# Performance work log

Hardware: AMD Instinct MI355X
Metric: run time of the kernel (lower is better)

## Reference

```python
import jax, jax.numpy as jnp
import numpy as np

N_NODES = 50000
N_EDGES = 800000
IN_C, HID_C, OUT_C = 128, 128, 64


def setup_inputs() -> dict:
    key = jax.random.key(0)
    k1, k2, k3, k4, k5 = jax.random.split(key, 5)
    x = jax.random.normal(k1, (N_NODES, IN_C), dtype=jnp.float32)
    edge_index = jax.random.randint(k2, (2, N_EDGES), 0, N_NODES, dtype=jnp.int64)
    # Glorot-style init for GCN weights, zero bias (PyG GCNConv defaults)
    s1 = (6.0 / (IN_C + HID_C)) ** 0.5
    s2 = (6.0 / (HID_C + OUT_C)) ** 0.5
    W1 = jax.random.uniform(k3, (IN_C, HID_C), jnp.float32, -s1, s1)
    W2 = jax.random.uniform(k4, (HID_C, OUT_C), jnp.float32, -s2, s2)
    b1 = jnp.zeros((HID_C,), jnp.float32)
    b2 = jnp.zeros((OUT_C,), jnp.float32)
    return {"x": x, "edge_index": edge_index, "W1": W1, "b1": b1, "W2": W2, "b2": b2}


def _gcn_conv(x, src, dst, W, b, n_nodes):
    # PyG GCNConv: add self-loops, symmetric normalization, linear transform,
    # scatter-add aggregation from src (row) to dst (col), then bias.
    h = x @ W  # [N, out]
    loops = jnp.arange(n_nodes, dtype=src.dtype)
    src_f = jnp.concatenate([src, loops])
    dst_f = jnp.concatenate([dst, loops])
    deg = jax.ops.segment_sum(jnp.ones_like(dst_f, dtype=h.dtype), dst_f,
                              num_segments=n_nodes)  # in-degree incl. self-loop
    dinv = jnp.where(deg > 0, jax.lax.rsqrt(deg), 0.0)
    norm = dinv[src_f] * dinv[dst_f]  # [E + N]
    msgs = h[src_f] * norm[:, None]   # gather + scale
    out = jax.ops.segment_sum(msgs, dst_f, num_segments=n_nodes)  # scatter-add
    return out + b


def reference(x, edge_index, W1, b1, W2, b2):
    src, dst = edge_index[0], edge_index[1]
    n = x.shape[0]
    h = jax.nn.relu(_gcn_conv(x, src, dst, W1, b1, n))
    return _gcn_conv(h, src, dst, W2, b2, n)
```

## Files before the change

### kernel.cpp

```cpp
#include <hip/hip_runtime.h>
#include <hip/hip_bf16.h>
#include <hip/hip_fp16.h>


#define NBUCK 800
#define CHUNK 2048
#define STASH 2048

typedef float f32x4 __attribute__((ext_vector_type(4)));
typedef _Float16 f16x8 __attribute__((ext_vector_type(8)));

__global__ __launch_bounds__(256) void presort_k(const int* __restrict__ src,
                                                 const int* __restrict__ dst,
                                                 unsigned* __restrict__ rec2,
                                                 int* __restrict__ hist2,
                                                 int* __restrict__ runstart2,
                                                 int E) {
    __shared__ int lh[NBUCK], lscan[NBUCK], cur[NBUCK];
    __shared__ int sred[256];
    __shared__ unsigned srec[CHUNK];
    int t = threadIdx.x;
    int lo = blockIdx.x * CHUNK, hi = min(E, lo + CHUNK);

    for (int i = t; i < NBUCK; i += 256) lh[i] = 0;
    __syncthreads();
    for (int e = lo + t; e < hi; e += 256)
        atomicAdd(&lh[dst[e] >> 6], 1);
    __syncthreads();

    int base = t * 4;
    int v[4];
    int s = 0;
#pragma unroll
    for (int i = 0; i < 4; ++i) {
        int idx = base + i;
        int c = (idx < NBUCK) ? lh[idx] : 0;
        v[i] = c; s += c;
    }
    sred[t] = s;
    __syncthreads();
#pragma unroll
    for (int off = 1; off < 256; off <<= 1) {
        int x = 0;
        if (t >= off) x = sred[t - off];
        __syncthreads();
        sred[t] += x;
        __syncthreads();
    }
    int run = sred[t] - s;
#pragma unroll
    for (int i = 0; i < 4; ++i) {
        int idx = base + i;
        if (idx < NBUCK) { lscan[idx] = run; cur[idx] = run; }
        run += v[i];
    }
    __syncthreads();

    for (int e = lo + t; e < hi; e += 256) {
        int d = dst[e];
        int p = atomicAdd(&cur[d >> 6], 1);
        srec[p] = (unsigned)(src[e] & 0xffff) | ((unsigned)d << 16);
    }
    __syncthreads();

    int n = hi - lo;
    for (int j = t; j < n; j += 256) rec2[lo + j] = srec[j];
    int hbase = blockIdx.x * NBUCK;
    for (int b = t; b < NBUCK; b += 256) {
        hist2[hbase + b] = lh[b];
        runstart2[hbase + b] = lscan[b];
    }
}

__global__ __launch_bounds__(256) void coltot_k(const int* __restrict__ hist2,
                                                int* __restrict__ btot, int BCNT) {
    __shared__ int sred[256];
    int b = blockIdx.x, t = threadIdx.x;
    int s = 0;
    for (int i = t; i < BCNT; i += 256) s += hist2[i * NBUCK + b];
    sred[t] = s;
    __syncthreads();
#pragma unroll
    for (int off = 128; off > 0; off >>= 1) {
        if (t < off) sred[t] += sred[t + off];
        __syncthreads();
    }
    if (t == 0) btot[b] = sred[0];
}

__global__ __launch_bounds__(256) void finish2_k(const unsigned* __restrict__ rec2,
                                                 const int* __restrict__ hist2,
                                                 const int* __restrict__ runstart2,
                                                 const int* __restrict__ btot,
                                                 int* __restrict__ offsets,
                                                 float* __restrict__ dinv,
                                                 unsigned short* __restrict__ adj,
                                                 int BCNT, int N, int E) {
    __shared__ int ncnt[64], ncur[64], nodeOff[64];
    __shared__ int stashCnt;
    __shared__ int sred[256];
    __shared__ unsigned stash[STASH];
    __shared__ unsigned short adjl[STASH];
    int b = blockIdx.x, t = threadIdx.x;
    if (t < 64) { ncnt[t] = 0; ncur[t] = 0; }
    if (t == 0) stashCnt = 0;
    if (b == 0 && t == 0) offsets[N] = E;

    int ps = 0;
    for (int i = t; i < b; i += 256) ps += btot[i];
    sred[t] = ps;
    __syncthreads();
#pragma unroll
    for (int off = 128; off > 0; off >>= 1) {
        if (t < off) sred[t] += sred[t + off];
        __syncthreads();
    }
    int bstart = sred[0];
    __syncthreads();

    for (int i = t; i < BCNT; i += 256) {
        int len = hist2[i * NBUCK + b];
        if (!len) continue;
        int gbase = i * CHUNK + runstart2[i * NBUCK + b];
        int sp = atomicAdd(&stashCnt, len);
        for (int k = 0; k < len; ++k) {
            unsigned r = rec2[gbase + k];
            atomicAdd(&ncnt[(r >> 16) & 63], 1);
            if (sp + k < STASH) stash[sp + k] = r;
        }
    }
    __syncthreads();

    if (t == 0) {
        int r = 0;
#pragma unroll
        for (int i = 0; i < 64; ++i) { nodeOff[i] = r; r += ncnt[i]; }
    }
    __syncthreads();

    if (t < 64) {
        int gnode = b * 64 + t;
        if (gnode < N) {
            dinv[gnode] = rsqrtf((float)(ncnt[t] + 1));
            offsets[gnode] = bstart + nodeOff[t];
        }
    }
    __syncthreads();

    int tot = stashCnt;
    if (tot > STASH) tot = STASH;
    for (int j = t; j < tot; j += 256) {
        unsigned r = stash[j];
        int ln = (r >> 16) & 63;
        int p = atomicAdd(&ncur[ln], 1);
        adjl[nodeOff[ln] + p] = (unsigned short)(r & 0xffff);
    }
    __syncthreads();
    for (int j = t; j < tot; j += 256) adj[bstart + j] = adjl[j];
}

template <int NOUT, bool HALF_IN>
__global__ __launch_bounds__(256) void gemm_mfma_k(const void* __restrict__ Xv,
                                                   const float* __restrict__ W,
                                                   const float* __restrict__ dinv,
                                                   __half* __restrict__ Hout, int M) {
    constexpr int K = 128;
    constexpr int BM = 64;
    constexpr int LDP = K + 8;
    constexpr int CT = NOUT / 16;
    __shared__ _Float16 xs[BM][LDP];
    __shared__ _Float16 wsl[NOUT][LDP];

    int t = threadIdx.x;
    int brow = blockIdx.x * BM;

    if constexpr (HALF_IN) {
        const __half* X = (const __half*)Xv;
        for (int i = t; i < BM * (K / 8); i += 256) {
            int row = i / (K / 8), c8 = i % (K / 8);
            int gr = brow + row;
            union { _Float16 h[8]; uint4 u; } pk;
            if (gr < M) {
                uint4 u = *(const uint4*)(X + (size_t)gr * K + c8 * 8);
                const __half2* hp = (const __half2*)&u;
                float di = dinv[gr];
#pragma unroll
                for (int j = 0; j < 4; ++j) {
                    float2 f = __half22float2(hp[j]);
                    pk.h[2 * j] = (_Float16)(f.x * di);
                    pk.h[2 * j + 1] = (_Float16)(f.y * di);
                }
            } else {
                pk.u = make_uint4(0, 0, 0, 0);
            }
            *(uint4*)&xs[row][c8 * 8] = pk.u;
        }
    } else {
        const float* X = (const float*)Xv;
        for (int i = t; i < BM * (K / 4); i += 256) {
            int row = i / (K / 4), c4 = i % (K / 4);
            int gr = brow + row;
            union { _Float16 h[4]; uint2 u; } pk;
            if (gr < M) {
                float4 v = *(const float4*)(X + (size_t)gr * K + c4 * 4);
                float di = dinv[gr];
                pk.h[0] = (_Float16)(v.x * di);
                pk.h[1] = (_Float16)(v.y * di);
                pk.h[2] = (_Float16)(v.z * di);
                pk.h[3] = (_Float16)(v.w * di);
            } else {
                pk.u = make_uint2(0, 0);
            }
            *(uint2*)&xs[row][c4 * 4] = pk.u;
        }
    }

    for (int i = t; i < K * (NOUT / 4); i += 256) {
        int k = i / (NOUT / 4), c4 = i % (NOUT / 4);
        float4 wv = *(const float4*)(W + (size_t)k * NOUT + c4 * 4);
        wsl[c4 * 4 + 0][k] = (_Float16)wv.x;
        wsl[c4 * 4 + 1][k] = (_Float16)wv.y;
        wsl[c4 * 4 + 2][k] = (_Float16)wv.z;
        wsl[c4 * 4 + 3][k] = (_Float16)wv.w;
    }
    __syncthreads();

    int w = t >> 6, lane = t & 63;
    int lrow = lane & 15;
    int lko = (lane >> 4) * 8;

    f32x4 acc[CT];
#pragma unroll
    for (int c = 0; c < CT; ++c) acc[c] = (f32x4){0.f, 0.f, 0.f, 0.f};

#pragma unroll
    for (int s = 0; s < K / 32; ++s) {
        f16x8 a = *(const f16x8*)&xs[w * 16 + lrow][s * 32 + lko];
#pragma unroll
        for (int c = 0; c < CT; ++c) {
            f16x8 b = *(const f16x8*)&wsl[c * 16 + lrow][s * 32 + lko];
            acc[c] = __builtin_amdgcn_mfma_f32_16x16x32_f16(a, b, acc[c], 0, 0, 0);
        }
    }

    __syncthreads();
#pragma unroll
    for (int c = 0; c < CT; ++c) {
#pragma unroll
        for (int r = 0; r < 4; ++r)
            xs[w * 16 + (lane >> 4) * 4 + r][c * 16 + lrow] = (_Float16)acc[c][r];
    }
    __syncthreads();
    for (int j = t; j < BM * (NOUT / 8); j += 256) {
        int row = j / (NOUT / 8), c8 = j % (NOUT / 8);
        int gr = brow + row;
        if (gr < M)
            *(uint4*)(Hout + (size_t)gr * NOUT + c8 * 8) = *(uint4*)&xs[row][c8 * 8];
    }
}

__device__ __forceinline__ void ld_row(const __half* p, float (&f)[4]) {
    uint2 u = *(const uint2*)p;
    const __half2* hp = (const __half2*)&u;
    float2 a = __half22float2(hp[0]);
    float2 b = __half22float2(hp[1]);
    f[0] = a.x; f[1] = a.y; f[2] = b.x; f[3] = b.y;
}
__device__ __forceinline__ void ld_row(const __half* p, float (&f)[2]) {
    float2 a = __half22float2(*(const __half2*)p);
    f[0] = a.x; f[1] = a.y;
}

template <int C, bool RELU, typename TOUT>
__global__ __launch_bounds__(256) void aggregate_k(const __half* __restrict__ H,
                                                   const int* __restrict__ offsets,
                                                   const unsigned short* __restrict__ adj,
                                                   const float* __restrict__ dinv,
                                                   const float* __restrict__ bias,
                                                   TOUT* __restrict__ out, int n) {
    constexpr int V = C / 32;
    int wave = threadIdx.x >> 6;
    int lane = threadIdx.x & 63;
    int half_id = lane >> 5;
    int sub = lane & 31;
    int node = blockIdx.x * 8 + wave * 2 + half_id;
    if (node >= n) return;

    const __half* hl = H + sub * V;

    float acc[V];
    ld_row(hl + (size_t)node * C, acc);

    int e0 = offsets[node], e1 = offsets[node + 1];
    int e = e0;

    for (; e + 8 <= e1; e += 8) {
        int s[8];
#pragma unroll
        for (int j = 0; j < 8; ++j) s[j] = adj[e + j];
        float t[8][V];
#pragma unroll
        for (int j = 0; j < 8; ++j) ld_row(hl + (size_t)s[j] * C, t[j]);
#pragma unroll
        for (int v = 0; v < V; ++v)
            acc[v] += ((t[0][v] + t[1][v]) + (t[2][v] + t[3][v])) +
                      ((t[4][v] + t[5][v]) + (t[6][v] + t[7][v]));
    }
    for (; e + 2 <= e1; e += 2) {
        int s0 = adj[e], s1 = adj[e + 1];
        float t0[V], t1[V];
        ld_row(hl + (size_t)s0 * C, t0);
        ld_row(hl + (size_t)s1 * C, t1);
#pragma unroll
        for (int v = 0; v < V; ++v) acc[v] += t0[v] + t1[v];
    }
    if (e < e1) {
        float t0[V];
        ld_row(hl + (size_t)adj[e] * C, t0);
#pragma unroll
        for (int v = 0; v < V; ++v) acc[v] += t0[v];
    }

    float di = dinv[node];
    float o[V];
#pragma unroll
    for (int v = 0; v < V; ++v) {
        o[v] = acc[v] * di + bias[sub * V + v];
        if (RELU) o[v] = fmaxf(o[v], 0.f);
    }

    if constexpr (sizeof(TOUT) == 2) {
        union { __half2 h[2]; uint2 u; } pk;
        pk.h[0] = __floats2half2_rn(o[0], o[1]);
        pk.h[1] = __floats2half2_rn(o[2], o[3]);
        *(uint2*)((__half*)out + (size_t)node * C + sub * V) = pk.u;
    } else {
        *(float2*)((float*)out + (size_t)node * C + sub * V) = make_float2(o[0], o[1]);
    }
}

extern "C" void kernel_launch(void* const* d_in, const int* in_sizes, int n_in,
                              void* d_out, int out_size, void* d_ws, size_t ws_size,
                              hipStream_t stream) {
    const float* x = (const float*)d_in[0];
    const int* ei = (const int*)d_in[1];
    const float* W1 = (const float*)d_in[2];
    const float* b1 = (const float*)d_in[3];
    const float* W2 = (const float*)d_in[4];
    const float* b2 = (const float*)d_in[5];
    float* out = (float*)d_out;

    const int IN_C = 128, HID_C = 128;
    int N = in_sizes[0] / IN_C;
    int E = in_sizes[1] / 2;
    const int* src = ei;
    const int* dst = ei + E;

    int BCNT = (E + CHUNK - 1) / CHUNK;

    int NP = (N + 255) & ~255;
    int EP = (E + 255) & ~255;
    char* w = (char*)d_ws;
    int* hist2 = (int*)w;           w += (size_t)BCNT * NBUCK * 4;
    int* runstart2 = (int*)w;       w += (size_t)BCNT * NBUCK * 4;
    int* btot = (int*)w;            w += (size_t)(NBUCK + 32) * 4;
    int* offsets = (int*)w;         w += (size_t)(NP + 256) * 4;
    float* dinv = (float*)w;        w += (size_t)NP * 4;
    unsigned* rec2 = (unsigned*)w;  w += (size_t)(BCNT * CHUNK) * 4;
    unsigned short* adj = (unsigned short*)w; w += (size_t)EP * 2;
    __half* H1 = (__half*)w;        w += (size_t)NP * HID_C * 2;
    __half* HID = (__half*)w;       w += (size_t)NP * HID_C * 2;
    (void)ws_size; (void)n_in; (void)out_size;

    presort_k<<<BCNT, 256, 0, stream>>>(src, dst, rec2, hist2, runstart2, E);
    coltot_k<<<NBUCK, 256, 0, stream>>>(hist2, btot, BCNT);
    finish2_k<<<NBUCK, 256, 0, stream>>>(rec2, hist2, runstart2, btot,
                                         offsets, dinv, adj, BCNT, N, E);

    gemm_mfma_k<128, false><<<(N + 63) / 64, 256, 0, stream>>>(x, W1, dinv, H1, N);
    aggregate_k<128, true, __half><<<(N + 7) / 8, 256, 0, stream>>>(
        H1, offsets, adj, dinv, b1, HID, N);

    gemm_mfma_k<64, true><<<(N + 63) / 64, 256, 0, stream>>>(HID, W2, dinv, H1, N);
    aggregate_k<64, false, float><<<(N + 7) / 8, 256, 0, stream>>>(
        H1, offsets, adj, dinv, b2, out, N);
}
```

Baseline: 121.7 us.

## Fuse layer-1 aggregation with layer-2 GEMM and pack presort tables

```diff
diff --git a/kernel.cpp b/kernel.cpp
--- a/kernel.cpp
+++ b/kernel.cpp
@@ -13,8 +13,7 @@
 __global__ __launch_bounds__(256) void presort_k(const int* __restrict__ src,
                                                  const int* __restrict__ dst,
                                                  unsigned* __restrict__ rec2,
-                                                 int* __restrict__ hist2,
-                                                 int* __restrict__ runstart2,
+                                                 unsigned* __restrict__ tab2,
                                                  int E) {
     __shared__ int lh[NBUCK], lscan[NBUCK], cur[NBUCK];
     __shared__ int sred[256];
@@ -66,18 +65,16 @@
     int n = hi - lo;
     for (int j = t; j < n; j += 256) rec2[lo + j] = srec[j];
     int hbase = blockIdx.x * NBUCK;
-    for (int b = t; b < NBUCK; b += 256) {
-        hist2[hbase + b] = lh[b];
-        runstart2[hbase + b] = lscan[b];
-    }
-}
-
-__global__ __launch_bounds__(256) void coltot_k(const int* __restrict__ hist2,
+    for (int b = t; b < NBUCK; b += 256)
+        tab2[hbase + b] = (unsigned)lh[b] | ((unsigned)lscan[b] << 16);
+}
+
+__global__ __launch_bounds__(256) void coltot_k(const unsigned* __restrict__ tab2,
                                                 int* __restrict__ btot, int BCNT) {
     __shared__ int sred[256];
     int b = blockIdx.x, t = threadIdx.x;
     int s = 0;
-    for (int i = t; i < BCNT; i += 256) s += hist2[i * NBUCK + b];
+    for (int i = t; i < BCNT; i += 256) s += (int)(tab2[i * NBUCK + b] & 0xffff);
     sred[t] = s;
     __syncthreads();
 #pragma unroll
@@ -89,8 +86,7 @@
 }
 
 __global__ __launch_bounds__(256) void finish2_k(const unsigned* __restrict__ rec2,
-                                                 const int* __restrict__ hist2,
-                                                 const int* __restrict__ runstart2,
+                                                 const unsigned* __restrict__ tab2,
                                                  const int* __restrict__ btot,
                                                  int* __restrict__ offsets,
                                                  float* __restrict__ dinv,
@@ -119,9 +115,10 @@
     __syncthreads();
 
     for (int i = t; i < BCNT; i += 256) {
-        int len = hist2[i * NBUCK + b];
+        unsigned h = tab2[i * NBUCK + b];
+        int len = (int)(h & 0xffff);
         if (!len) continue;
-        int gbase = i * CHUNK + runstart2[i * NBUCK + b];
+        int gbase = i * CHUNK + (int)(h >> 16);
         int sp = atomicAdd(&stashCnt, len);
         for (int k = 0; k < len; ++k) {
             unsigned r = rec2[gbase + k];
@@ -159,8 +156,8 @@
     for (int j = t; j < tot; j += 256) adj[bstart + j] = adjl[j];
 }
 
-template <int NOUT, bool HALF_IN>
-__global__ __launch_bounds__(256) void gemm_mfma_k(const void* __restrict__ Xv,
+template <int NOUT>
+__global__ __launch_bounds__(256) void gemm_mfma_k(const float* __restrict__ X,
                                                    const float* __restrict__ W,
                                                    const float* __restrict__ dinv,
                                                    __half* __restrict__ Hout, int M) {
@@ -174,45 +171,21 @@
     int t = threadIdx.x;
     int brow = blockIdx.x * BM;
 
-    if constexpr (HALF_IN) {
-        const __half* X = (const __half*)Xv;
-        for (int i = t; i < BM * (K / 8); i += 256) {
-            int row = i / (K / 8), c8 = i % (K / 8);
-            int gr = brow + row;
-            union { _Float16 h[8]; uint4 u; } pk;
-            if (gr < M) {
-                uint4 u = *(const uint4*)(X + (size_t)gr * K + c8 * 8);
-                const __half2* hp = (const __half2*)&u;
-                float di = dinv[gr];
-#pragma unroll
-                for (int j = 0; j < 4; ++j) {
-                    float2 f = __half22float2(hp[j]);
-                    pk.h[2 * j] = (_Float16)(f.x * di);
-                    pk.h[2 * j + 1] = (_Float16)(f.y * di);
-                }
-            } else {
-                pk.u = make_uint4(0, 0, 0, 0);
-            }
-            *(uint4*)&xs[row][c8 * 8] = pk.u;
-        }
-    } else {
-        const float* X = (const float*)Xv;
-        for (int i = t; i < BM * (K / 4); i += 256) {
-            int row = i / (K / 4), c4 = i % (K / 4);
-            int gr = brow + row;
-            union { _Float16 h[4]; uint2 u; } pk;
-            if (gr < M) {
-                float4 v = *(const float4*)(X + (size_t)gr * K + c4 * 4);
-                float di = dinv[gr];
-                pk.h[0] = (_Float16)(v.x * di);
-                pk.h[1] = (_Float16)(v.y * di);
-                pk.h[2] = (_Float16)(v.z * di);
-                pk.h[3] = (_Float16)(v.w * di);
-            } else {
-                pk.u = make_uint2(0, 0);
-            }
-            *(uint2*)&xs[row][c4 * 4] = pk.u;
-        }
+    for (int i = t; i < BM * (K / 4); i += 256) {
+        int row = i / (K / 4), c4 = i % (K / 4);
+        int gr = brow + row;
+        union { _Float16 h[4]; uint2 u; } pk;
+        if (gr < M) {
+            float4 v = *(const float4*)(X + (size_t)gr * K + c4 * 4);
+            float di = dinv[gr];
+            pk.h[0] = (_Float16)(v.x * di);
+            pk.h[1] = (_Float16)(v.y * di);
+            pk.h[2] = (_Float16)(v.z * di);
+            pk.h[3] = (_Float16)(v.w * di);
+        } else {
+            pk.u = make_uint2(0, 0);
+        }
+        *(uint2*)&xs[row][c4 * 4] = pk.u;
     }
 
     for (int i = t; i < K * (NOUT / 4); i += 256) {
@@ -271,14 +244,130 @@
     f[0] = a.x; f[1] = a.y;
 }
 
-template <int C, bool RELU, typename TOUT>
-__global__ __launch_bounds__(256) void aggregate_k(const __half* __restrict__ H,
-                                                   const int* __restrict__ offsets,
-                                                   const unsigned short* __restrict__ adj,
-                                                   const float* __restrict__ dinv,
-                                                   const float* __restrict__ bias,
-                                                   TOUT* __restrict__ out, int n) {
-    constexpr int V = C / 32;
+__device__ __forceinline__ void agg_edges(const __half* __restrict__ hl,
+                                          const unsigned short* __restrict__ adj,
+                                          int e0, int e1, float (&acc)[4]) {
+    int e = e0;
+    for (; e + 8 <= e1; e += 8) {
+        int s[8];
+#pragma unroll
+        for (int j = 0; j < 8; ++j) s[j] = adj[e + j];
+        float t[8][4];
+#pragma unroll
+        for (int j = 0; j < 8; ++j) ld_row(hl + (size_t)s[j] * 128, t[j]);
+#pragma unroll
+        for (int v = 0; v < 4; ++v)
+            acc[v] += ((t[0][v] + t[1][v]) + (t[2][v] + t[3][v])) +
+                      ((t[4][v] + t[5][v]) + (t[6][v] + t[7][v]));
+    }
+    for (; e + 2 <= e1; e += 2) {
+        int s0 = adj[e], s1 = adj[e + 1];
+        float t0[4], t1[4];
+        ld_row(hl + (size_t)s0 * 128, t0);
+        ld_row(hl + (size_t)s1 * 128, t1);
+#pragma unroll
+        for (int v = 0; v < 4; ++v) acc[v] += t0[v] + t1[v];
+    }
+    if (e < e1) {
+        float t0[4];
+        ld_row(hl + (size_t)adj[e] * 128, t0);
+#pragma unroll
+        for (int v = 0; v < 4; ++v) acc[v] += t0[v];
+    }
+}
+
+template <int NOUT>
+__global__ __launch_bounds__(256) void agg_gemm_k(const __half* __restrict__ H,
+                                                  const int* __restrict__ offsets,
+                                                  const unsigned short* __restrict__ adj,
+                                                  const float* __restrict__ dinv,
+                                                  const float* __restrict__ b1,
+                                                  const float* __restrict__ W,
+                                                  __half* __restrict__ Hout, int N) {
+    constexpr int K = 128;
+    constexpr int LDP = K + 8;
+    constexpr int CT = NOUT / 16;
+    __shared__ _Float16 xs[64][LDP];
+    __shared__ _Float16 wsl[NOUT][LDP];
+
+    int t = threadIdx.x;
+    int brow = blockIdx.x * 64;
+
+    for (int i = t; i < K * (NOUT / 4); i += 256) {
+        int k = i / (NOUT / 4), c4 = i % (NOUT / 4);
+        float4 wv = *(const float4*)(W + (size_t)k * NOUT + c4 * 4);
+        wsl[c4 * 4 + 0][k] = (_Float16)wv.x;
+        wsl[c4 * 4 + 1][k] = (_Float16)wv.y;
+        wsl[c4 * 4 + 2][k] = (_Float16)wv.z;
+        wsl[c4 * 4 + 3][k] = (_Float16)wv.w;
+    }
+
+    int hw = t >> 5, sub = t & 31;
+    const __half* hl = H + sub * 4;
+#pragma unroll 1
+    for (int r = 0; r < 8; ++r) {
+        int lr = r * 8 + hw;
+        int node = brow + lr;
+        union { _Float16 h[4]; uint2 u; } pk;
+        if (node < N) {
+            float acc[4];
+            ld_row(hl + (size_t)node * 128, acc);
+            agg_edges(hl, adj, offsets[node], offsets[node + 1], acc);
+            float di = dinv[node];
+#pragma unroll
+            for (int v = 0; v < 4; ++v) {
+                float o = acc[v] * di + b1[sub * 4 + v];
+                o = fmaxf(o, 0.f);
+                pk.h[v] = (_Float16)(o * di);
+            }
+        } else {
+            pk.u = make_uint2(0, 0);
+        }
+        *(uint2*)&xs[lr][sub * 4] = pk.u;
+    }
+    __syncthreads();
+
+    int w = t >> 6, lane = t & 63;
+    int lrow = lane & 15;
+    int lko = (lane >> 4) * 8;
+
+    f32x4 acc[CT];
+#pragma unroll
+    for (int c = 0; c < CT; ++c) acc[c] = (f32x4){0.f, 0.f, 0.f, 0.f};
+
+#pragma unroll
+    for (int s = 0; s < K / 32; ++s) {
+        f16x8 a = *(const f16x8*)&xs[w * 16 + lrow][s * 32 + lko];
+#pragma unroll
+        for (int c = 0; c < CT; ++c) {
+            f16x8 b = *(const f16x8*)&wsl[c * 16 + lrow][s * 32 + lko];
+            acc[c] = __builtin_amdgcn_mfma_f32_16x16x32_f16(a, b, acc[c], 0, 0, 0);
+        }
+    }
+
+    __syncthreads();
+#pragma unroll
+    for (int c = 0; c < CT; ++c) {
+#pragma unroll
+        for (int r = 0; r < 4; ++r)
+            xs[w * 16 + (lane >> 4) * 4 + r][c * 16 + lrow] = (_Float16)acc[c][r];
+    }
+    __syncthreads();
+    for (int j = t; j < 64 * (NOUT / 8); j += 256) {
+        int row = j / (NOUT / 8), c8 = j % (NOUT / 8);
+        int gr = brow + row;
+        if (gr < N)
+            *(uint4*)(Hout + (size_t)gr * NOUT + c8 * 8) = *(uint4*)&xs[row][c8 * 8];
+    }
+}
+
+__global__ __launch_bounds__(256) void aggregate2_k(const __half* __restrict__ H,
+                                                    const int* __restrict__ offsets,
+                                                    const unsigned short* __restrict__ adj,
+                                                    const float* __restrict__ dinv,
+                                                    const float* __restrict__ bias,
+                                                    float* __restrict__ out, int n) {
+    constexpr int C = 64, V = 2;
     int wave = threadIdx.x >> 6;
     int lane = threadIdx.x & 63;
     int half_id = lane >> 5;
@@ -293,7 +382,6 @@
 
     int e0 = offsets[node], e1 = offsets[node + 1];
     int e = e0;
-
     for (; e + 8 <= e1; e += 8) {
         int s[8];
 #pragma unroll
@@ -322,21 +410,9 @@
     }
 
     float di = dinv[node];
-    float o[V];
-#pragma unroll
-    for (int v = 0; v < V; ++v) {
-        o[v] = acc[v] * di + bias[sub * V + v];
-        if (RELU) o[v] = fmaxf(o[v], 0.f);
-    }
-
-    if constexpr (sizeof(TOUT) == 2) {
-        union { __half2 h[2]; uint2 u; } pk;
-        pk.h[0] = __floats2half2_rn(o[0], o[1]);
-        pk.h[1] = __floats2half2_rn(o[2], o[3]);
-        *(uint2*)((__half*)out + (size_t)node * C + sub * V) = pk.u;
-    } else {
-        *(float2*)((float*)out + (size_t)node * C + sub * V) = make_float2(o[0], o[1]);
-    }
+    float o0 = acc[0] * di + bias[sub * V + 0];
+    float o1 = acc[1] * di + bias[sub * V + 1];
+    *(float2*)(out + (size_t)node * C + sub * V) = make_float2(o0, o1);
 }
 
 extern "C" void kernel_launch(void* const* d_in, const int* in_sizes, int n_in,
@@ -350,7 +426,7 @@
     const float* b2 = (const float*)d_in[5];
     float* out = (float*)d_out;
 
-    const int IN_C = 128, HID_C = 128;
+    const int IN_C = 128, HID_C = 128, OUT_C = 64;
     int N = in_sizes[0] / IN_C;
     int E = in_sizes[1] / 2;
     const int* src = ei;
@@ -361,27 +437,26 @@
     int NP = (N + 255) & ~255;
     int EP = (E + 255) & ~255;
     char* w = (char*)d_ws;
-    int* hist2 = (int*)w;           w += (size_t)BCNT * NBUCK * 4;
-    int* runstart2 = (int*)w;       w += (size_t)BCNT * NBUCK * 4;
+    unsigned* tab2 = (unsigned*)w;  w += (size_t)BCNT * NBUCK * 4;
     int* btot = (int*)w;            w += (size_t)(NBUCK + 32) * 4;
     int* offsets = (int*)w;         w += (size_t)(NP + 256) * 4;
     float* dinv = (float*)w;        w += (size_t)NP * 4;
     unsigned* rec2 = (unsigned*)w;  w += (size_t)(BCNT * CHUNK) * 4;
     unsigned short* adj = (unsigned short*)w; w += (size_t)EP * 2;
     __half* H1 = (__half*)w;        w += (size_t)NP * HID_C * 2;
-    __half* HID = (__half*)w;       w += (size_t)NP * HID_C * 2;
+    __half* H2 = (__half*)w;        w += (size_t)NP * OUT_C * 2;
     (void)ws_size; (void)n_in; (void)out_size;
 
-    presort_k<<<BCNT, 256, 0, stream>>>(src, dst, rec2, hist2, runstart2, E);
-    coltot_k<<<NBUCK, 256, 0, stream>>>(hist2, btot, BCNT);
-    finish2_k<<<NBUCK, 256, 0, stream>>>(rec2, hist2, runstart2, btot,
+    presort_k<<<BCNT, 256, 0, stream>>>(src, dst, rec2, tab2, E);
+    coltot_k<<<NBUCK, 256, 0, stream>>>(tab2, btot, BCNT);
+    finish2_k<<<NBUCK, 256, 0, stream>>>(rec2, tab2, btot,
                                          offsets, dinv, adj, BCNT, N, E);
 
-    gemm_mfma_k<128, false><<<(N + 63) / 64, 256, 0, stream>>>(x, W1, dinv, H1, N);
-    aggregate_k<128, true, __half><<<(N + 7) / 8, 256, 0, stream>>>(
-        H1, offsets, adj, dinv, b1, HID, N);
-
-    gemm_mfma_k<64, true><<<(N + 63) / 64, 256, 0, stream>>>(HID, W2, dinv, H1, N);
-    aggregate_k<64, false, float><<<(N + 7) / 8, 256, 0, stream>>>(
-        H1, offsets, adj, dinv, b2, out, N);
-}
+    gemm_mfma_k<128><<<(N + 63) / 64, 256, 0, stream>>>(x, W1, dinv, H1, N);
+
+    agg_gemm_k<64><<<(N + 63) / 64, 256, 0, stream>>>(
+        H1, offsets, adj, dinv, b1, W2, H2, N);
+
+    aggregate2_k<<<(N + 7) / 8, 256, 0, stream>>>(
+        H2, offsets, adj, dinv, b2, out, N);
+}
```

Result: slower. 125.8 us (+3.3%).
